# Performance work log

Hardware: AMD Instinct MI355X
Metric: run time of the kernel (lower is better)

The kernel has to match this reference:

```python
import jax, jax.numpy as jnp
import numpy as np

H, W, D = 64, 96, 64          # matching_height, matching_width, num_depth_bins
B, V, C = 1, 4, 16            # batch, num_src_frames, matching feature channels
EPS = 1e-8                    # Project3D eps


def setup_inputs() -> dict:
    key = jax.random.key(0)
    k0, k1, k2 = jax.random.split(key, 3)
    cur_feats = jax.random.normal(k0, (B, C, H, W), jnp.float32)
    src_feats = jax.random.normal(k1, (B, V, C, H, W), jnp.float32)
    # realistic pinhole intrinsics (4x4 homogeneous)
    K = np.eye(4, dtype=np.float32)
    K[0, 0], K[1, 1], K[0, 2], K[1, 2] = 0.9 * W, 1.2 * H, W / 2.0, H / 2.0
    src_Ks = jnp.broadcast_to(jnp.asarray(K), (B, V, 4, 4))
    cur_invK = jnp.broadcast_to(jnp.asarray(np.linalg.inv(K)), (B, 4, 4))
    # near-identity extrinsics (cur cam -> src cam) with small random translations
    t = jax.random.normal(k2, (B, V, 3), jnp.float32) * 0.1
    E = jnp.broadcast_to(jnp.eye(4, dtype=jnp.float32), (B, V, 4, 4))
    src_extrinsics = E.at[:, :, :3, 3].set(t)
    min_depth = jnp.full((B, 1, 1, 1), 0.25, jnp.float32)
    max_depth = jnp.full((B, 1, 1, 1), 5.0, jnp.float32)
    return dict(cur_feats=cur_feats, src_feats=src_feats,
                src_extrinsics=src_extrinsics, src_Ks=src_Ks,
                cur_invK=cur_invK, min_depth=min_depth, max_depth=max_depth)


def _grid_sample_zeros(feat_chw, x, y):
    """torch.grid_sample(mode='bilinear', padding_mode='zeros', align_corners=False)
    for one image. feat_chw: (C,H,W); x,y: (M,) un-normalized pixel coords."""
    f = feat_chw.reshape(feat_chw.shape[0], H * W)  # (C, HW)
    x0, y0 = jnp.floor(x), jnp.floor(y)
    out = jnp.zeros((f.shape[0], x.shape[0]), f.dtype)
    for dx in (0.0, 1.0):
        for dy in (0.0, 1.0):
            xi, yi = x0 + dx, y0 + dy
            w = (1.0 - jnp.abs(x - xi)) * (1.0 - jnp.abs(y - yi))
            valid = (xi >= 0) & (xi < W) & (yi >= 0) & (yi < H)
            idx = (jnp.clip(yi, 0, H - 1) * W + jnp.clip(xi, 0, W - 1)).astype(jnp.int32)
            out = out + f[:, idx] * (w * jnp.where(valid, 1.0, 0.0))[None]
    return out  # (C, M)


def reference(cur_feats, src_feats, src_extrinsics, src_Ks, cur_invK, min_depth, max_depth):
    N = H * W
    # --- generate_depth_planes (log_plane=False -> linear in inverse depth) ---
    ramp = jnp.linspace(0.0, 1.0, D).reshape(1, D)              # linear_ramp
    inv_min = 1.0 / min_depth.reshape(B, 1)
    inv_max = 1.0 / max_depth.reshape(B, 1)
    depth_planes_bd = 1.0 / (inv_min + (inv_max - inv_min) * ramp)  # (B, D)

    # --- BackprojectDepth: pixel grid (+0.5), rays = invK[:3,:3] @ pix ---
    xx, yy = jnp.meshgrid(jnp.arange(W, dtype=jnp.float32) + 0.5,
                          jnp.arange(H, dtype=jnp.float32) + 0.5)
    pix_3N = jnp.stack([xx.ravel(), yy.ravel(), jnp.ones(N, jnp.float32)], 0)
    rays_b3N = jnp.einsum('bij,jn->bin', cur_invK[:, :3, :3], pix_3N)
    world_bd3N = rays_b3N[:, None] * depth_planes_bd[:, :, None, None]   # (B,D,3,N)
    world_bd4N = jnp.concatenate(
        [world_bd3N, jnp.ones((B, D, 1, N), world_bd3N.dtype)], axis=2)

    # --- Project3D: P = K @ T; pix = cam[:2]/(cam[2]+eps) ---
    P_bv34 = jnp.einsum('bvij,bvjk->bvik', src_Ks, src_extrinsics)[:, :, :3]
    cam = jnp.einsum('bvij,bdjn->bvdin', P_bv34, world_bd4N)             # (B,V,D,3,N)
    z = cam[:, :, :, 2]                                                  # (B,V,D,N)
    u = cam[:, :, :, 0] / (z + EPS)
    v = cam[:, :, :, 1] / (z + EPS)

    # uv normalization then grid_sample unnormalization (align_corners=False)
    un = 2.0 * u * (1.0 / W) - 1.0
    vn = 2.0 * v * (1.0 / H) - 1.0
    x = (un + 1.0) * W / 2.0 - 0.5
    y = (vn + 1.0) * H / 2.0 - 0.5

    warped = jax.vmap(_grid_sample_zeros)(
        src_feats.reshape(B * V, C, H, W),
        x.reshape(B * V, D * N), y.reshape(B * V, D * N))                # (BV,C,DN)
    warped = warped.reshape(B, V, C, D, H, W)

    mask = (z > 0).astype(warped.dtype).reshape(B, V, D, H, W)
    # dot over channels with current features, mask, sum over source views
    dot_bvdhw = jnp.einsum('bvcdhw,bchw->bvdhw', warped, cur_feats) * mask
    cost_volume = dot_bvdhw.sum(axis=1)                                  # (B,D,H,W)
    return cost_volume
```

## Files before the change

### kernel.cpp

```cpp
#include <hip/hip_runtime.h>
#include <hip/hip_fp16.h>

#define HH 64
#define WW 96
#define DD 64
#define VV 4
#define CC 16
#define HW (HH*WW)
#define EPSF 1e-8f

typedef _Float16 half2_t __attribute__((ext_vector_type(2)));

#if defined(__has_builtin)
#if __has_builtin(__builtin_amdgcn_fdot2)
#define HAVE_FDOT2 1
#endif
#endif

__device__ __forceinline__ float fdot2_acc(half2_t a, half2_t b, float c) {
#ifdef HAVE_FDOT2
    return __builtin_amdgcn_fdot2(a, b, c, false);
#else
    return c + (float)a.x * (float)b.x + (float)a.y * (float)b.y;
#endif
}

__global__ __launch_bounds__(256) void cv_pack_kernel(
    const float* __restrict__ src, const float* __restrict__ cur,
    __half* __restrict__ srcT, __half* __restrict__ curT)
{
    int tid = blockIdx.x * blockDim.x + threadIdx.x;
    if (tid < VV * HW) {
        int v  = tid / HW;
        int hw = tid - v * HW;
        unsigned short pk[CC];
        #pragma unroll
        for (int c = 0; c < CC; ++c) {
            float f = src[(size_t)v * CC * HW + c * HW + hw];
            pk[c] = __half_as_ushort(__float2half(f));
        }
        uint4* dst = (uint4*)(srcT + (size_t)tid * CC);
        dst[0] = *(uint4*)&pk[0];
        dst[1] = *(uint4*)&pk[8];
    } else {
        int hw = tid - VV * HW;
        if (hw < HW) {
            unsigned short pk[CC];
            #pragma unroll
            for (int c = 0; c < CC; ++c) {
                float f = cur[c * HW + hw];
                pk[c] = __half_as_ushort(__float2half(f));
            }
            uint4* dst = (uint4*)(curT + (size_t)hw * CC);
            dst[0] = *(uint4*)&pk[0];
            dst[1] = *(uint4*)&pk[8];
        }
    }
}

__device__ __forceinline__ float tap_dot16(const __half* __restrict__ p,
                                           const half2_t* __restrict__ cf2)
{
    half2_t hv[8];
    const uint4* q = (const uint4*)p;
    *(uint4*)&hv[0] = q[0];
    *(uint4*)&hv[4] = q[1];
    float s = 0.f;
    #pragma unroll
    for (int i = 0; i < 8; ++i)
        s = fdot2_acc(hv[i], cf2[i], s);
    return s;
}

__global__ __launch_bounds__(256) void cost_volume_f16_kernel(
    const __half* __restrict__ curT,
    const __half* __restrict__ srcT,
    const float* __restrict__ extr,
    const float* __restrict__ Ks,
    const float* __restrict__ invK,
    const float* __restrict__ min_d,
    const float* __restrict__ max_d,
    float* __restrict__ out)
{
    __shared__ float P_s[VV * 12];
    {
        int t = threadIdx.x;
        if (t < VV * 12) {
            int v   = t / 12;
            int r   = (t % 12) / 4;
            int col = t % 4;
            float s = 0.f;
            #pragma unroll
            for (int k = 0; k < 4; ++k)
                s += Ks[v * 16 + r * 4 + k] * extr[v * 16 + k * 4 + col];
            P_s[t] = s;
        }
    }
    __syncthreads();

    int tid = blockIdx.x * blockDim.x + threadIdx.x;
    if (tid >= DD * HW) return;
    int d  = tid / HW;
    int hw = tid - d * HW;
    int h  = hw / WW;
    int w  = hw - h * WW;

    float px = (float)w + 0.5f, py = (float)h + 0.5f;
    float rx = invK[0] * px + invK[1] * py + invK[2];
    float ry = invK[4] * px + invK[5] * py + invK[6];
    float rz = invK[8] * px + invK[9] * py + invK[10];

    float inv_min = 1.f / min_d[0];
    float inv_max = 1.f / max_d[0];
    float depth   = 1.f / (inv_min + (inv_max - inv_min) * ((float)d / (float)(DD - 1)));

    half2_t cf2[8];
    {
        const uint4* p = (const uint4*)(curT + (size_t)hw * CC);
        *(uint4*)&cf2[0] = p[0];
        *(uint4*)&cf2[4] = p[1];
    }

    float acc = 0.f;
    #pragma unroll
    for (int v = 0; v < VV; ++v) {
        const float* P = &P_s[v * 12];
        float cx = depth * (P[0] * rx + P[1] * ry + P[2]  * rz) + P[3];
        float cy = depth * (P[4] * rx + P[5] * ry + P[6]  * rz) + P[7];
        float cz = depth * (P[8] * rx + P[9] * ry + P[10] * rz) + P[11];
        if (cz > 0.f) {
            float iz = 1.f / (cz + EPSF);
            float x = cx * iz - 0.5f;
            float y = cy * iz - 0.5f;
            float x0f = floorf(x), y0f = floorf(y);
            float fx = x - x0f, fy = y - y0f;
            float x1f = x0f + 1.f, y1f = y0f + 1.f;
            int ix0 = (int)fminf(fmaxf(x0f, 0.f), (float)(WW - 1));
            int ix1 = (int)fminf(fmaxf(x1f, 0.f), (float)(WW - 1));
            int iy0 = (int)fminf(fmaxf(y0f, 0.f), (float)(HH - 1));
            int iy1 = (int)fminf(fmaxf(y1f, 0.f), (float)(HH - 1));
            bool vx0 = (x0f >= 0.f) && (x0f < (float)WW);
            bool vx1 = (x1f >= 0.f) && (x1f < (float)WW);
            bool vy0 = (y0f >= 0.f) && (y0f < (float)HH);
            bool vy1 = (y1f >= 0.f) && (y1f < (float)HH);
            float w00 = (vx0 && vy0) ? (1.f - fx) * (1.f - fy) : 0.f;
            float w01 = (vx1 && vy0) ? fx * (1.f - fy) : 0.f;
            float w10 = (vx0 && vy1) ? (1.f - fx) * fy : 0.f;
            float w11 = (vx1 && vy1) ? fx * fy : 0.f;

            const __half* base = srcT + (size_t)v * HW * CC;
            float d00 = tap_dot16(base + (size_t)(iy0 * WW + ix0) * CC, cf2);
            float d01 = tap_dot16(base + (size_t)(iy0 * WW + ix1) * CC, cf2);
            float d10 = tap_dot16(base + (size_t)(iy1 * WW + ix0) * CC, cf2);
            float d11 = tap_dot16(base + (size_t)(iy1 * WW + ix1) * CC, cf2);

            acc += w00 * d00 + w01 * d01 + w10 * d10 + w11 * d11;
        }
    }
    out[tid] = acc;
}

__global__ __launch_bounds__(256) void cost_volume_fallback_kernel(
    const float* __restrict__ curF,
    const float* __restrict__ srcF,
    const float* __restrict__ extr,
    const float* __restrict__ Ks,
    const float* __restrict__ invK,
    const float* __restrict__ min_d,
    const float* __restrict__ max_d,
    float* __restrict__ out)
{
    __shared__ float P_s[VV * 12];
    {
        int t = threadIdx.x;
        if (t < VV * 12) {
            int v   = t / 12;
            int r   = (t % 12) / 4;
            int col = t % 4;
            float s = 0.f;
            #pragma unroll
            for (int k = 0; k < 4; ++k)
                s += Ks[v * 16 + r * 4 + k] * extr[v * 16 + k * 4 + col];
            P_s[t] = s;
        }
    }
    __syncthreads();

    int tid = blockIdx.x * blockDim.x + threadIdx.x;
    if (tid >= DD * HW) return;
    int d  = tid / HW;
    int hw = tid - d * HW;
    int h  = hw / WW;
    int w  = hw - h * WW;

    float px = (float)w + 0.5f, py = (float)h + 0.5f;
    float rx = invK[0] * px + invK[1] * py + invK[2];
    float ry = invK[4] * px + invK[5] * py + invK[6];
    float rz = invK[8] * px + invK[9] * py + invK[10];

    float inv_min = 1.f / min_d[0];
    float inv_max = 1.f / max_d[0];
    float depth   = 1.f / (inv_min + (inv_max - inv_min) * ((float)d / (float)(DD - 1)));

    float cf[CC];
    #pragma unroll
    for (int c = 0; c < CC; ++c) cf[c] = curF[c * HW + hw];

    float acc = 0.f;
    #pragma unroll
    for (int v = 0; v < VV; ++v) {
        const float* P = &P_s[v * 12];
        float cx = depth * (P[0] * rx + P[1] * ry + P[2]  * rz) + P[3];
        float cy = depth * (P[4] * rx + P[5] * ry + P[6]  * rz) + P[7];
        float cz = depth * (P[8] * rx + P[9] * ry + P[10] * rz) + P[11];
        if (cz > 0.f) {
            float iz = 1.f / (cz + EPSF);
            float x = cx * iz - 0.5f;
            float y = cy * iz - 0.5f;
            float x0f = floorf(x), y0f = floorf(y);
            float fx = x - x0f, fy = y - y0f;
            float x1f = x0f + 1.f, y1f = y0f + 1.f;
            int ix0 = (int)fminf(fmaxf(x0f, 0.f), (float)(WW - 1));
            int ix1 = (int)fminf(fmaxf(x1f, 0.f), (float)(WW - 1));
            int iy0 = (int)fminf(fmaxf(y0f, 0.f), (float)(HH - 1));
            int iy1 = (int)fminf(fmaxf(y1f, 0.f), (float)(HH - 1));
            bool vx0 = (x0f >= 0.f) && (x0f < (float)WW);
            bool vx1 = (x1f >= 0.f) && (x1f < (float)WW);
            bool vy0 = (y0f >= 0.f) && (y0f < (float)HH);
            bool vy1 = (y1f >= 0.f) && (y1f < (float)HH);
            float w00 = (vx0 && vy0) ? (1.f - fx) * (1.f - fy) : 0.f;
            float w01 = (vx1 && vy0) ? fx * (1.f - fy) : 0.f;
            float w10 = (vx0 && vy1) ? (1.f - fx) * fy : 0.f;
            float w11 = (vx1 && vy1) ? fx * fy : 0.f;

            float d00 = 0.f, d01 = 0.f, d10 = 0.f, d11 = 0.f;
            int b = v * CC * HW;
            int i00 = iy0 * WW + ix0, i01 = iy0 * WW + ix1;
            int i10 = iy1 * WW + ix0, i11 = iy1 * WW + ix1;
            #pragma unroll
            for (int c = 0; c < CC; ++c) {
                const float* fc = srcF + b + c * HW;
                d00 += fc[i00] * cf[c];
                d01 += fc[i01] * cf[c];
                d10 += fc[i10] * cf[c];
                d11 += fc[i11] * cf[c];
            }
            acc += w00 * d00 + w01 * d01 + w10 * d10 + w11 * d11;
        }
    }
    out[tid] = acc;
}

extern "C" void kernel_launch(void* const* d_in, const int* in_sizes, int n_in,
                              void* d_out, int out_size, void* d_ws, size_t ws_size,
                              hipStream_t stream) {
    const float* cur  = (const float*)d_in[0];
    const float* src  = (const float*)d_in[1];
    const float* extr = (const float*)d_in[2];
    const float* Ks   = (const float*)d_in[3];
    const float* invK = (const float*)d_in[4];
    const float* mind = (const float*)d_in[5];
    const float* maxd = (const float*)d_in[6];
    float* out = (float*)d_out;

    const size_t need = (size_t)(VV * HW * CC + HW * CC) * sizeof(__half);
    const int n_out  = DD * HW;
    const int blocks = (n_out + 255) / 256;

    if (ws_size >= need) {
        __half* srcT = (__half*)d_ws;
        __half* curT = srcT + (size_t)VV * HW * CC;
        const int total = VV * HW + HW;
        cv_pack_kernel<<<(total + 255) / 256, 256, 0, stream>>>(src, cur, srcT, curT);
        cost_volume_f16_kernel<<<blocks, 256, 0, stream>>>(
            curT, srcT, extr, Ks, invK, mind, maxd, out);
    } else {
        cost_volume_fallback_kernel<<<blocks, 256, 0, stream>>>(
            cur, src, extr, Ks, invK, mind, maxd, out);
    }
}
```

Baseline: 76.03 us.

## Process four depth planes per thread to reuse per-pixel setup and current features

Each thread now handles one pixel across four consecutive depth bins, so the ray, the per-view projection terms and the current-feature load are computed once and reused. The block size drops to 128 threads and the grid is re-indexed by depth group and pixel tile. Reciprocals switch to the fast hardware rcp intrinsic, and the cz>0 test becomes a select rather than a branch, so every tap is gathered even for points behind the camera. The trade-offs are higher register pressure, fewer threads in flight, and slightly less precise reciprocals.

```diff
diff --git a/kernel.cpp b/kernel.cpp
--- a/kernel.cpp
+++ b/kernel.cpp
@@ -8,6 +8,9 @@
 #define CC 16
 #define HW (HH*WW)
 #define EPSF 1e-8f
+
+#define DPT 4
+#define MBLK 128
 
 typedef _Float16 half2_t __attribute__((ext_vector_type(2)));
 
@@ -72,7 +75,7 @@
     return s;
 }
 
-__global__ __launch_bounds__(256) void cost_volume_f16_kernel(
+__global__ __launch_bounds__(MBLK) void cost_volume_f16_kernel(
     const __half* __restrict__ curT,
     const __half* __restrict__ srcT,
     const float* __restrict__ extr,
@@ -98,6 +101,111 @@
     }
     __syncthreads();
 
+    const int dg = blockIdx.x / (HW / MBLK);
+    const int hw = (blockIdx.x % (HW / MBLK)) * MBLK + threadIdx.x;
+    const int h  = hw / WW;
+    const int w  = hw - h * WW;
+
+    float px = (float)w + 0.5f, py = (float)h + 0.5f;
+    float rx = invK[0] * px + invK[1] * py + invK[2];
+    float ry = invK[4] * px + invK[5] * py + invK[6];
+    float rz = invK[8] * px + invK[9] * py + invK[10];
+
+    float inv_min = __builtin_amdgcn_rcpf(min_d[0]);
+    float inv_max = __builtin_amdgcn_rcpf(max_d[0]);
+    float dmm = inv_max - inv_min;
+
+    float dep[DPT];
+    #pragma unroll
+    for (int i = 0; i < DPT; ++i) {
+        float fd = (float)(dg * DPT + i) * (1.f / (float)(DD - 1));
+        dep[i] = __builtin_amdgcn_rcpf(inv_min + dmm * fd);
+    }
+
+    half2_t cf2[8];
+    {
+        const uint4* p = (const uint4*)(curT + (size_t)hw * CC);
+        *(uint4*)&cf2[0] = p[0];
+        *(uint4*)&cf2[4] = p[1];
+    }
+
+    float acc[DPT];
+    #pragma unroll
+    for (int i = 0; i < DPT; ++i) acc[i] = 0.f;
+
+    #pragma unroll
+    for (int v = 0; v < VV; ++v) {
+        const float* P = &P_s[v * 12];
+        float a = P[0] * rx + P[1] * ry + P[2]  * rz;
+        float b = P[4] * rx + P[5] * ry + P[6]  * rz;
+        float c = P[8] * rx + P[9] * ry + P[10] * rz;
+        const __half* base = srcT + (size_t)v * HW * CC;
+
+        #pragma unroll
+        for (int i = 0; i < DPT; ++i) {
+            float cz = dep[i] * c + P[11];
+            float cx = dep[i] * a + P[3];
+            float cy = dep[i] * b + P[7];
+            float iz = __builtin_amdgcn_rcpf(cz + EPSF);
+            float x = cx * iz - 0.5f;
+            float y = cy * iz - 0.5f;
+            float x0f = floorf(x), y0f = floorf(y);
+            float fx = x - x0f, fy = y - y0f;
+            float x1f = x0f + 1.f, y1f = y0f + 1.f;
+            int ix0 = (int)fminf(fmaxf(x0f, 0.f), (float)(WW - 1));
+            int ix1 = (int)fminf(fmaxf(x1f, 0.f), (float)(WW - 1));
+            int iy0 = (int)fminf(fmaxf(y0f, 0.f), (float)(HH - 1));
+            int iy1 = (int)fminf(fmaxf(y1f, 0.f), (float)(HH - 1));
+            bool vx0 = (x0f >= 0.f) && (x0f < (float)WW);
+            bool vx1 = (x1f >= 0.f) && (x1f < (float)WW);
+            bool vy0 = (y0f >= 0.f) && (y0f < (float)HH);
+            bool vy1 = (y1f >= 0.f) && (y1f < (float)HH);
+            float w00 = (vx0 && vy0) ? (1.f - fx) * (1.f - fy) : 0.f;
+            float w01 = (vx1 && vy0) ? fx * (1.f - fy) : 0.f;
+            float w10 = (vx0 && vy1) ? (1.f - fx) * fy : 0.f;
+            float w11 = (vx1 && vy1) ? fx * fy : 0.f;
+
+            float d00 = tap_dot16(base + (size_t)(iy0 * WW + ix0) * CC, cf2);
+            float d01 = tap_dot16(base + (size_t)(iy0 * WW + ix1) * CC, cf2);
+            float d10 = tap_dot16(base + (size_t)(iy1 * WW + ix0) * CC, cf2);
+            float d11 = tap_dot16(base + (size_t)(iy1 * WW + ix1) * CC, cf2);
+
+            float vacc = w00 * d00 + w01 * d01 + w10 * d10 + w11 * d11;
+            acc[i] += (cz > 0.f) ? vacc : 0.f;
+        }
+    }
+
+    #pragma unroll
+    for (int i = 0; i < DPT; ++i)
+        out[(size_t)(dg * DPT + i) * HW + hw] = acc[i];
+}
+
+__global__ __launch_bounds__(256) void cost_volume_fallback_kernel(
+    const float* __restrict__ curF,
+    const float* __restrict__ srcF,
+    const float* __restrict__ extr,
+    const float* __restrict__ Ks,
+    const float* __restrict__ invK,
+    const float* __restrict__ min_d,
+    const float* __restrict__ max_d,
+    float* __restrict__ out)
+{
+    __shared__ float P_s[VV * 12];
+    {
+        int t = threadIdx.x;
+        if (t < VV * 12) {
+            int v   = t / 12;
+            int r   = (t % 12) / 4;
+            int col = t % 4;
+            float s = 0.f;
+            #pragma unroll
+            for (int k = 0; k < 4; ++k)
+                s += Ks[v * 16 + r * 4 + k] * extr[v * 16 + k * 4 + col];
+            P_s[t] = s;
+        }
+    }
+    __syncthreads();
+
     int tid = blockIdx.x * blockDim.x + threadIdx.x;
     if (tid >= DD * HW) return;
     int d  = tid / HW;
@@ -114,12 +222,9 @@
     float inv_max = 1.f / max_d[0];
     float depth   = 1.f / (inv_min + (inv_max - inv_min) * ((float)d / (float)(DD - 1)));
 
-    half2_t cf2[8];
-    {
-        const uint4* p = (const uint4*)(curT + (size_t)hw * CC);
-        *(uint4*)&cf2[0] = p[0];
-        *(uint4*)&cf2[4] = p[1];
-    }
+    float cf[CC];
+    #pragma unroll
+    for (int c = 0; c < CC; ++c) cf[c] = curF[c * HW + hw];
 
     float acc = 0.f;
     #pragma unroll
@@ -148,91 +253,6 @@
             float w10 = (vx0 && vy1) ? (1.f - fx) * fy : 0.f;
             float w11 = (vx1 && vy1) ? fx * fy : 0.f;
 
-            const __half* base = srcT + (size_t)v * HW * CC;
-            float d00 = tap_dot16(base + (size_t)(iy0 * WW + ix0) * CC, cf2);
-            float d01 = tap_dot16(base + (size_t)(iy0 * WW + ix1) * CC, cf2);
-            float d10 = tap_dot16(base + (size_t)(iy1 * WW + ix0) * CC, cf2);
-            float d11 = tap_dot16(base + (size_t)(iy1 * WW + ix1) * CC, cf2);
-
-            acc += w00 * d00 + w01 * d01 + w10 * d10 + w11 * d11;
-        }
-    }
-    out[tid] = acc;
-}
-
-__global__ __launch_bounds__(256) void cost_volume_fallback_kernel(
-    const float* __restrict__ curF,
-    const float* __restrict__ srcF,
-    const float* __restrict__ extr,
-    const float* __restrict__ Ks,
-    const float* __restrict__ invK,
-    const float* __restrict__ min_d,
-    const float* __restrict__ max_d,
-    float* __restrict__ out)
-{
-    __shared__ float P_s[VV * 12];
-    {
-        int t = threadIdx.x;
-        if (t < VV * 12) {
-            int v   = t / 12;
-            int r   = (t % 12) / 4;
-            int col = t % 4;
-            float s = 0.f;
-            #pragma unroll
-            for (int k = 0; k < 4; ++k)
-                s += Ks[v * 16 + r * 4 + k] * extr[v * 16 + k * 4 + col];
-            P_s[t] = s;
-        }
-    }
-    __syncthreads();
-
-    int tid = blockIdx.x * blockDim.x + threadIdx.x;
-    if (tid >= DD * HW) return;
-    int d  = tid / HW;
-    int hw = tid - d * HW;
-    int h  = hw / WW;
-    int w  = hw - h * WW;
-
-    float px = (float)w + 0.5f, py = (float)h + 0.5f;
-    float rx = invK[0] * px + invK[1] * py + invK[2];
-    float ry = invK[4] * px + invK[5] * py + invK[6];
-    float rz = invK[8] * px + invK[9] * py + invK[10];
-
-    float inv_min = 1.f / min_d[0];
-    float inv_max = 1.f / max_d[0];
-    float depth   = 1.f / (inv_min + (inv_max - inv_min) * ((float)d / (float)(DD - 1)));
-
-    float cf[CC];
-    #pragma unroll
-    for (int c = 0; c < CC; ++c) cf[c] = curF[c * HW + hw];
-
-    float acc = 0.f;
-    #pragma unroll
-    for (int v = 0; v < VV; ++v) {
-        const float* P = &P_s[v * 12];
-        float cx = depth * (P[0] * rx + P[1] * ry + P[2]  * rz) + P[3];
-        float cy = depth * (P[4] * rx + P[5] * ry + P[6]  * rz) + P[7];
-        float cz = depth * (P[8] * rx + P[9] * ry + P[10] * rz) + P[11];
-        if (cz > 0.f) {
-            float iz = 1.f / (cz + EPSF);
-            float x = cx * iz - 0.5f;
-            float y = cy * iz - 0.5f;
-            float x0f = floorf(x), y0f = floorf(y);
-            float fx = x - x0f, fy = y - y0f;
-            float x1f = x0f + 1.f, y1f = y0f + 1.f;
-            int ix0 = (int)fminf(fmaxf(x0f, 0.f), (float)(WW - 1));
-            int ix1 = (int)fminf(fmaxf(x1f, 0.f), (float)(WW - 1));
-            int iy0 = (int)fminf(fmaxf(y0f, 0.f), (float)(HH - 1));
-            int iy1 = (int)fminf(fmaxf(y1f, 0.f), (float)(HH - 1));
-            bool vx0 = (x0f >= 0.f) && (x0f < (float)WW);
-            bool vx1 = (x1f >= 0.f) && (x1f < (float)WW);
-            bool vy0 = (y0f >= 0.f) && (y0f < (float)HH);
-            bool vy1 = (y1f >= 0.f) && (y1f < (float)HH);
-            float w00 = (vx0 && vy0) ? (1.f - fx) * (1.f - fy) : 0.f;
-            float w01 = (vx1 && vy0) ? fx * (1.f - fy) : 0.f;
-            float w10 = (vx0 && vy1) ? (1.f - fx) * fy : 0.f;
-            float w11 = (vx1 && vy1) ? fx * fy : 0.f;
-
             float d00 = 0.f, d01 = 0.f, d10 = 0.f, d11 = 0.f;
             int b = v * CC * HW;
             int i00 = iy0 * WW + ix0, i01 = iy0 * WW + ix1;
@@ -265,16 +285,17 @@
 
     const size_t need = (size_t)(VV * HW * CC + HW * CC) * sizeof(__half);
     const int n_out  = DD * HW;
-    const int blocks = (n_out + 255) / 256;
 
     if (ws_size >= need) {
         __half* srcT = (__half*)d_ws;
         __half* curT = srcT + (size_t)VV * HW * CC;
         const int total = VV * HW + HW;
         cv_pack_kernel<<<(total + 255) / 256, 256, 0, stream>>>(src, cur, srcT, curT);
-        cost_volume_f16_kernel<<<blocks, 256, 0, stream>>>(
+        const int mblocks = (DD / DPT) * (HW / MBLK);
+        cost_volume_f16_kernel<<<mblocks, MBLK, 0, stream>>>(
             curT, srcT, extr, Ks, invK, mind, maxd, out);
     } else {
+        const int blocks = (n_out + 255) / 256;
         cost_volume_fallback_kernel<<<blocks, 256, 0, stream>>>(
             cur, src, extr, Ks, invK, mind, maxd, out);
     }
```

Result: slower. 81.82 us (+7.6%).

## Map wavefront lanes to depth bins per pixel in f16 cost volume kernel

Applied to the files above, without the earlier changes.

Reassigns threads so each 64-lane wavefront handles one pixel and its lanes cover the 64 depth bins, instead of consecutive pixels at one depth. All lanes then share the current-feature load and ray computation, and the gathered source taps of neighbouring depths cluster along the epipolar line. The cost is output writes strided by HW, which are no longer coalesced. It also swaps divisions for hardware reciprocal approximations and replaces the cz>0 branch with a predicated select to avoid divergence, so all four taps are always fetched.

```diff
diff --git a/kernel.cpp b/kernel.cpp
--- a/kernel.cpp
+++ b/kernel.cpp
@@ -8,6 +8,8 @@
 #define CC 16
 #define HW (HH*WW)
 #define EPSF 1e-8f
+
+#define PIX_PER_BLOCK 4
 
 typedef _Float16 half2_t __attribute__((ext_vector_type(2)));
 
@@ -98,6 +100,100 @@
     }
     __syncthreads();
 
+    const int wv   = threadIdx.x >> 6;
+    const int lane = threadIdx.x & 63;
+    const int hw   = blockIdx.x * PIX_PER_BLOCK + wv;
+    const int h    = hw / WW;
+    const int w    = hw - h * WW;
+    const int d    = lane;
+
+    float px = (float)w + 0.5f, py = (float)h + 0.5f;
+    float rx = invK[0] * px + invK[1] * py + invK[2];
+    float ry = invK[4] * px + invK[5] * py + invK[6];
+    float rz = invK[8] * px + invK[9] * py + invK[10];
+
+    float inv_min = __builtin_amdgcn_rcpf(min_d[0]);
+    float inv_max = __builtin_amdgcn_rcpf(max_d[0]);
+    float depth = __builtin_amdgcn_rcpf(
+        inv_min + (inv_max - inv_min) * ((float)d * (1.f / (float)(DD - 1))));
+
+    half2_t cf2[8];
+    {
+        const uint4* p = (const uint4*)(curT + (size_t)hw * CC);
+        *(uint4*)&cf2[0] = p[0];
+        *(uint4*)&cf2[4] = p[1];
+    }
+
+    float acc = 0.f;
+    #pragma unroll
+    for (int v = 0; v < VV; ++v) {
+        const float* P = &P_s[v * 12];
+        float a = P[0] * rx + P[1] * ry + P[2]  * rz;
+        float b = P[4] * rx + P[5] * ry + P[6]  * rz;
+        float c = P[8] * rx + P[9] * ry + P[10] * rz;
+
+        float cx = depth * a + P[3];
+        float cy = depth * b + P[7];
+        float cz = depth * c + P[11];
+
+        float iz = __builtin_amdgcn_rcpf(cz + EPSF);
+        float x = cx * iz - 0.5f;
+        float y = cy * iz - 0.5f;
+        float x0f = floorf(x), y0f = floorf(y);
+        float fx = x - x0f, fy = y - y0f;
+        float x1f = x0f + 1.f, y1f = y0f + 1.f;
+        int ix0 = (int)fminf(fmaxf(x0f, 0.f), (float)(WW - 1));
+        int ix1 = (int)fminf(fmaxf(x1f, 0.f), (float)(WW - 1));
+        int iy0 = (int)fminf(fmaxf(y0f, 0.f), (float)(HH - 1));
+        int iy1 = (int)fminf(fmaxf(y1f, 0.f), (float)(HH - 1));
+        bool vx0 = (x0f >= 0.f) && (x0f < (float)WW);
+        bool vx1 = (x1f >= 0.f) && (x1f < (float)WW);
+        bool vy0 = (y0f >= 0.f) && (y0f < (float)HH);
+        bool vy1 = (y1f >= 0.f) && (y1f < (float)HH);
+        float w00 = (vx0 && vy0) ? (1.f - fx) * (1.f - fy) : 0.f;
+        float w01 = (vx1 && vy0) ? fx * (1.f - fy) : 0.f;
+        float w10 = (vx0 && vy1) ? (1.f - fx) * fy : 0.f;
+        float w11 = (vx1 && vy1) ? fx * fy : 0.f;
+
+        const __half* base = srcT + (size_t)v * HW * CC;
+        float d00 = tap_dot16(base + (size_t)(iy0 * WW + ix0) * CC, cf2);
+        float d01 = tap_dot16(base + (size_t)(iy0 * WW + ix1) * CC, cf2);
+        float d10 = tap_dot16(base + (size_t)(iy1 * WW + ix0) * CC, cf2);
+        float d11 = tap_dot16(base + (size_t)(iy1 * WW + ix1) * CC, cf2);
+
+        float vacc = w00 * d00 + w01 * d01 + w10 * d10 + w11 * d11;
+        acc += (cz > 0.f) ? vacc : 0.f;
+    }
+
+    out[(size_t)d * HW + hw] = acc;
+}
+
+__global__ __launch_bounds__(256) void cost_volume_fallback_kernel(
+    const float* __restrict__ curF,
+    const float* __restrict__ srcF,
+    const float* __restrict__ extr,
+    const float* __restrict__ Ks,
+    const float* __restrict__ invK,
+    const float* __restrict__ min_d,
+    const float* __restrict__ max_d,
+    float* __restrict__ out)
+{
+    __shared__ float P_s[VV * 12];
+    {
+        int t = threadIdx.x;
+        if (t < VV * 12) {
+            int v   = t / 12;
+            int r   = (t % 12) / 4;
+            int col = t % 4;
+            float s = 0.f;
+            #pragma unroll
+            for (int k = 0; k < 4; ++k)
+                s += Ks[v * 16 + r * 4 + k] * extr[v * 16 + k * 4 + col];
+            P_s[t] = s;
+        }
+    }
+    __syncthreads();
+
     int tid = blockIdx.x * blockDim.x + threadIdx.x;
     if (tid >= DD * HW) return;
     int d  = tid / HW;
@@ -114,12 +210,9 @@
     float inv_max = 1.f / max_d[0];
     float depth   = 1.f / (inv_min + (inv_max - inv_min) * ((float)d / (float)(DD - 1)));
 
-    half2_t cf2[8];
-    {
-        const uint4* p = (const uint4*)(curT + (size_t)hw * CC);
-        *(uint4*)&cf2[0] = p[0];
-        *(uint4*)&cf2[4] = p[1];
-    }
+    float cf[CC];
+    #pragma unroll
+    for (int c = 0; c < CC; ++c) cf[c] = curF[c * HW + hw];
 
     float acc = 0.f;
     #pragma unroll
@@ -148,91 +241,6 @@
             float w10 = (vx0 && vy1) ? (1.f - fx) * fy : 0.f;
             float w11 = (vx1 && vy1) ? fx * fy : 0.f;
 
-            const __half* base = srcT + (size_t)v * HW * CC;
-            float d00 = tap_dot16(base + (size_t)(iy0 * WW + ix0) * CC, cf2);
-            float d01 = tap_dot16(base + (size_t)(iy0 * WW + ix1) * CC, cf2);
-            float d10 = tap_dot16(base + (size_t)(iy1 * WW + ix0) * CC, cf2);
-            float d11 = tap_dot16(base + (size_t)(iy1 * WW + ix1) * CC, cf2);
-
-            acc += w00 * d00 + w01 * d01 + w10 * d10 + w11 * d11;
-        }
-    }
-    out[tid] = acc;
-}
-
-__global__ __launch_bounds__(256) void cost_volume_fallback_kernel(
-    const float* __restrict__ curF,
-    const float* __restrict__ srcF,
-    const float* __restrict__ extr,
-    const float* __restrict__ Ks,
-    const float* __restrict__ invK,
-    const float* __restrict__ min_d,
-    const float* __restrict__ max_d,
-    float* __restrict__ out)
-{
-    __shared__ float P_s[VV * 12];
-    {
-        int t = threadIdx.x;
-        if (t < VV * 12) {
-            int v   = t / 12;
-            int r   = (t % 12) / 4;
-            int col = t % 4;
-            float s = 0.f;
-            #pragma unroll
-            for (int k = 0; k < 4; ++k)
-                s += Ks[v * 16 + r * 4 + k] * extr[v * 16 + k * 4 + col];
-            P_s[t] = s;
-        }
-    }
-    __syncthreads();
-
-    int tid = blockIdx.x * blockDim.x + threadIdx.x;
-    if (tid >= DD * HW) return;
-    int d  = tid / HW;
-    int hw = tid - d * HW;
-    int h  = hw / WW;
-    int w  = hw - h * WW;
-
-    float px = (float)w + 0.5f, py = (float)h + 0.5f;
-    float rx = invK[0] * px + invK[1] * py + invK[2];
-    float ry = invK[4] * px + invK[5] * py + invK[6];
-    float rz = invK[8] * px + invK[9] * py + invK[10];
-
-    float inv_min = 1.f / min_d[0];
-    float inv_max = 1.f / max_d[0];
-    float depth   = 1.f / (inv_min + (inv_max - inv_min) * ((float)d / (float)(DD - 1)));
-
-    float cf[CC];
-    #pragma unroll
-    for (int c = 0; c < CC; ++c) cf[c] = curF[c * HW + hw];
-
-    float acc = 0.f;
-    #pragma unroll
-    for (int v = 0; v < VV; ++v) {
-        const float* P = &P_s[v * 12];
-        float cx = depth * (P[0] * rx + P[1] * ry + P[2]  * rz) + P[3];
-        float cy = depth * (P[4] * rx + P[5] * ry + P[6]  * rz) + P[7];
-        float cz = depth * (P[8] * rx + P[9] * ry + P[10] * rz) + P[11];
-        if (cz > 0.f) {
-            float iz = 1.f / (cz + EPSF);
-            float x = cx * iz - 0.5f;
-            float y = cy * iz - 0.5f;
-            float x0f = floorf(x), y0f = floorf(y);
-            float fx = x - x0f, fy = y - y0f;
-            float x1f = x0f + 1.f, y1f = y0f + 1.f;
-            int ix0 = (int)fminf(fmaxf(x0f, 0.f), (float)(WW - 1));
-            int ix1 = (int)fminf(fmaxf(x1f, 0.f), (float)(WW - 1));
-            int iy0 = (int)fminf(fmaxf(y0f, 0.f), (float)(HH - 1));
-            int iy1 = (int)fminf(fmaxf(y1f, 0.f), (float)(HH - 1));
-            bool vx0 = (x0f >= 0.f) && (x0f < (float)WW);
-            bool vx1 = (x1f >= 0.f) && (x1f < (float)WW);
-            bool vy0 = (y0f >= 0.f) && (y0f < (float)HH);
-            bool vy1 = (y1f >= 0.f) && (y1f < (float)HH);
-            float w00 = (vx0 && vy0) ? (1.f - fx) * (1.f - fy) : 0.f;
-            float w01 = (vx1 && vy0) ? fx * (1.f - fy) : 0.f;
-            float w10 = (vx0 && vy1) ? (1.f - fx) * fy : 0.f;
-            float w11 = (vx1 && vy1) ? fx * fy : 0.f;
-
             float d00 = 0.f, d01 = 0.f, d10 = 0.f, d11 = 0.f;
             int b = v * CC * HW;
             int i00 = iy0 * WW + ix0, i01 = iy0 * WW + ix1;
@@ -265,16 +273,17 @@
 
     const size_t need = (size_t)(VV * HW * CC + HW * CC) * sizeof(__half);
     const int n_out  = DD * HW;
-    const int blocks = (n_out + 255) / 256;
 
     if (ws_size >= need) {
         __half* srcT = (__half*)d_ws;
         __half* curT = srcT + (size_t)VV * HW * CC;
         const int total = VV * HW + HW;
         cv_pack_kernel<<<(total + 255) / 256, 256, 0, stream>>>(src, cur, srcT, curT);
-        cost_volume_f16_kernel<<<blocks, 256, 0, stream>>>(
+        const int mblocks = HW / PIX_PER_BLOCK;
+        cost_volume_f16_kernel<<<mblocks, 256, 0, stream>>>(
             curT, srcT, extr, Ks, invK, mind, maxd, out);
     } else {
+        const int blocks = (n_out + 255) / 256;
         cost_volume_fallback_kernel<<<blocks, 256, 0, stream>>>(
             cur, src, extr, Ks, invK, mind, maxd, out);
     }
```

After: 79.12 us. 1.04x slower.

## Split channel dot across two lanes per output and use fast reciprocals

Applied to the files above, without the earlier changes.

The fp16 cost-volume kernel now assigns two threads to each output, each handling 8 of the 16 channels, and combines them with a lane shuffle. The goal is more parallelism and smaller per-thread gathers (one 16-byte load per tap instead of two), which should help hide the latency of the random bilinear taps. Exact divisions are also replaced with hardware approximate reciprocals. In exchange, the projection and weight math is duplicated across both lanes, there are twice as many threads, and the reciprocals are slightly less precise.

```diff
diff --git a/kernel.cpp b/kernel.cpp
--- a/kernel.cpp
+++ b/kernel.cpp
@@ -58,16 +58,14 @@
     }
 }
 
-__device__ __forceinline__ float tap_dot16(const __half* __restrict__ p,
-                                           const half2_t* __restrict__ cf2)
-{
-    half2_t hv[8];
-    const uint4* q = (const uint4*)p;
-    *(uint4*)&hv[0] = q[0];
-    *(uint4*)&hv[4] = q[1];
+__device__ __forceinline__ float tap_dot8(const __half* __restrict__ p,
+                                          const half2_t* __restrict__ cf2)
+{
+    half2_t hv[4];
+    *(uint4*)&hv[0] = *(const uint4*)p;
     float s = 0.f;
     #pragma unroll
-    for (int i = 0; i < 8; ++i)
+    for (int i = 0; i < 4; ++i)
         s = fdot2_acc(hv[i], cf2[i], s);
     return s;
 }
@@ -98,6 +96,98 @@
     }
     __syncthreads();
 
+    const int tid2    = blockIdx.x * blockDim.x + threadIdx.x;
+    const int out_idx = tid2 >> 1;
+    const int half    = tid2 & 1;
+    const int d  = out_idx / HW;
+    const int hw = out_idx - d * HW;
+    const int h  = hw / WW;
+    const int w  = hw - h * WW;
+
+    float px = (float)w + 0.5f, py = (float)h + 0.5f;
+    float rx = invK[0] * px + invK[1] * py + invK[2];
+    float ry = invK[4] * px + invK[5] * py + invK[6];
+    float rz = invK[8] * px + invK[9] * py + invK[10];
+
+    float inv_min = __builtin_amdgcn_rcpf(min_d[0]);
+    float inv_max = __builtin_amdgcn_rcpf(max_d[0]);
+    float depth = __builtin_amdgcn_rcpf(
+        inv_min + (inv_max - inv_min) * ((float)d * (1.f / (float)(DD - 1))));
+
+    half2_t cf2[4];
+    {
+        const uint4* p = (const uint4*)(curT + (size_t)hw * CC + half * 8);
+        *(uint4*)&cf2[0] = *p;
+    }
+
+    float acc = 0.f;
+    #pragma unroll
+    for (int v = 0; v < VV; ++v) {
+        const float* P = &P_s[v * 12];
+        float cx = depth * (P[0] * rx + P[1] * ry + P[2]  * rz) + P[3];
+        float cy = depth * (P[4] * rx + P[5] * ry + P[6]  * rz) + P[7];
+        float cz = depth * (P[8] * rx + P[9] * ry + P[10] * rz) + P[11];
+        if (cz > 0.f) {
+            float iz = __builtin_amdgcn_rcpf(cz + EPSF);
+            float x = cx * iz - 0.5f;
+            float y = cy * iz - 0.5f;
+            float x0f = floorf(x), y0f = floorf(y);
+            float fx = x - x0f, fy = y - y0f;
+            float x1f = x0f + 1.f, y1f = y0f + 1.f;
+            int ix0 = (int)fminf(fmaxf(x0f, 0.f), (float)(WW - 1));
+            int ix1 = (int)fminf(fmaxf(x1f, 0.f), (float)(WW - 1));
+            int iy0 = (int)fminf(fmaxf(y0f, 0.f), (float)(HH - 1));
+            int iy1 = (int)fminf(fmaxf(y1f, 0.f), (float)(HH - 1));
+            bool vx0 = (x0f >= 0.f) && (x0f < (float)WW);
+            bool vx1 = (x1f >= 0.f) && (x1f < (float)WW);
+            bool vy0 = (y0f >= 0.f) && (y0f < (float)HH);
+            bool vy1 = (y1f >= 0.f) && (y1f < (float)HH);
+            float w00 = (vx0 && vy0) ? (1.f - fx) * (1.f - fy) : 0.f;
+            float w01 = (vx1 && vy0) ? fx * (1.f - fy) : 0.f;
+            float w10 = (vx0 && vy1) ? (1.f - fx) * fy : 0.f;
+            float w11 = (vx1 && vy1) ? fx * fy : 0.f;
+
+            const __half* base = srcT + (size_t)v * HW * CC + half * 8;
+            float d00 = tap_dot8(base + (size_t)(iy0 * WW + ix0) * CC, cf2);
+            float d01 = tap_dot8(base + (size_t)(iy0 * WW + ix1) * CC, cf2);
+            float d10 = tap_dot8(base + (size_t)(iy1 * WW + ix0) * CC, cf2);
+            float d11 = tap_dot8(base + (size_t)(iy1 * WW + ix1) * CC, cf2);
+
+            acc += w00 * d00 + w01 * d01 + w10 * d10 + w11 * d11;
+        }
+    }
+
+    acc += __shfl_xor(acc, 1, 64);
+    if (half == 0)
+        out[out_idx] = acc;
+}
+
+__global__ __launch_bounds__(256) void cost_volume_fallback_kernel(
+    const float* __restrict__ curF,
+    const float* __restrict__ srcF,
+    const float* __restrict__ extr,
+    const float* __restrict__ Ks,
+    const float* __restrict__ invK,
+    const float* __restrict__ min_d,
+    const float* __restrict__ max_d,
+    float* __restrict__ out)
+{
+    __shared__ float P_s[VV * 12];
+    {
+        int t = threadIdx.x;
+        if (t < VV * 12) {
+            int v   = t / 12;
+            int r   = (t % 12) / 4;
+            int col = t % 4;
+            float s = 0.f;
+            #pragma unroll
+            for (int k = 0; k < 4; ++k)
+                s += Ks[v * 16 + r * 4 + k] * extr[v * 16 + k * 4 + col];
+            P_s[t] = s;
+        }
+    }
+    __syncthreads();
+
     int tid = blockIdx.x * blockDim.x + threadIdx.x;
     if (tid >= DD * HW) return;
     int d  = tid / HW;
@@ -114,12 +204,9 @@
     float inv_max = 1.f / max_d[0];
     float depth   = 1.f / (inv_min + (inv_max - inv_min) * ((float)d / (float)(DD - 1)));
 
-    half2_t cf2[8];
-    {
-        const uint4* p = (const uint4*)(curT + (size_t)hw * CC);
-        *(uint4*)&cf2[0] = p[0];
-        *(uint4*)&cf2[4] = p[1];
-    }
+    float cf[CC];
+    #pragma unroll
+    for (int c = 0; c < CC; ++c) cf[c] = curF[c * HW + hw];
 
     float acc = 0.f;
     #pragma unroll
@@ -148,91 +235,6 @@
             float w10 = (vx0 && vy1) ? (1.f - fx) * fy : 0.f;
             float w11 = (vx1 && vy1) ? fx * fy : 0.f;
 
-            const __half* base = srcT + (size_t)v * HW * CC;
-            float d00 = tap_dot16(base + (size_t)(iy0 * WW + ix0) * CC, cf2);
-            float d01 = tap_dot16(base + (size_t)(iy0 * WW + ix1) * CC, cf2);
-            float d10 = tap_dot16(base + (size_t)(iy1 * WW + ix0) * CC, cf2);
-            float d11 = tap_dot16(base + (size_t)(iy1 * WW + ix1) * CC, cf2);
-
-            acc += w00 * d00 + w01 * d01 + w10 * d10 + w11 * d11;
-        }
-    }
-    out[tid] = acc;
-}
-
-__global__ __launch_bounds__(256) void cost_volume_fallback_kernel(
-    const float* __restrict__ curF,
-    const float* __restrict__ srcF,
-    const float* __restrict__ extr,
-    const float* __restrict__ Ks,
-    const float* __restrict__ invK,
-    const float* __restrict__ min_d,
-    const float* __restrict__ max_d,
-    float* __restrict__ out)
-{
-    __shared__ float P_s[VV * 12];
-    {
-        int t = threadIdx.x;
-        if (t < VV * 12) {
-            int v   = t / 12;
-            int r   = (t % 12) / 4;
-            int col = t % 4;
-            float s = 0.f;
-            #pragma unroll
-            for (int k = 0; k < 4; ++k)
-                s += Ks[v * 16 + r * 4 + k] * extr[v * 16 + k * 4 + col];
-            P_s[t] = s;
-        }
-    }
-    __syncthreads();
-
-    int tid = blockIdx.x * blockDim.x + threadIdx.x;
-    if (tid >= DD * HW) return;
-    int d  = tid / HW;
-    int hw = tid - d * HW;
-    int h  = hw / WW;
-    int w  = hw - h * WW;
-
-    float px = (float)w + 0.5f, py = (float)h + 0.5f;
-    float rx = invK[0] * px + invK[1] * py + invK[2];
-    float ry = invK[4] * px + invK[5] * py + invK[6];
-    float rz = invK[8] * px + invK[9] * py + invK[10];
-
-    float inv_min = 1.f / min_d[0];
-    float inv_max = 1.f / max_d[0];
-    float depth   = 1.f / (inv_min + (inv_max - inv_min) * ((float)d / (float)(DD - 1)));
-
-    float cf[CC];
-    #pragma unroll
-    for (int c = 0; c < CC; ++c) cf[c] = curF[c * HW + hw];
-
-    float acc = 0.f;
-    #pragma unroll
-    for (int v = 0; v < VV; ++v) {
-        const float* P = &P_s[v * 12];
-        float cx = depth * (P[0] * rx + P[1] * ry + P[2]  * rz) + P[3];
-        float cy = depth * (P[4] * rx + P[5] * ry + P[6]  * rz) + P[7];
-        float cz = depth * (P[8] * rx + P[9] * ry + P[10] * rz) + P[11];
-        if (cz > 0.f) {
-            float iz = 1.f / (cz + EPSF);
-            float x = cx * iz - 0.5f;
-            float y = cy * iz - 0.5f;
-            float x0f = floorf(x), y0f = floorf(y);
-            float fx = x - x0f, fy = y - y0f;
-            float x1f = x0f + 1.f, y1f = y0f + 1.f;
-            int ix0 = (int)fminf(fmaxf(x0f, 0.f), (float)(WW - 1));
-            int ix1 = (int)fminf(fmaxf(x1f, 0.f), (float)(WW - 1));
-            int iy0 = (int)fminf(fmaxf(y0f, 0.f), (float)(HH - 1));
-            int iy1 = (int)fminf(fmaxf(y1f, 0.f), (float)(HH - 1));
-            bool vx0 = (x0f >= 0.f) && (x0f < (float)WW);
-            bool vx1 = (x1f >= 0.f) && (x1f < (float)WW);
-            bool vy0 = (y0f >= 0.f) && (y0f < (float)HH);
-            bool vy1 = (y1f >= 0.f) && (y1f < (float)HH);
-            float w00 = (vx0 && vy0) ? (1.f - fx) * (1.f - fy) : 0.f;
-            float w01 = (vx1 && vy0) ? fx * (1.f - fy) : 0.f;
-            float w10 = (vx0 && vy1) ? (1.f - fx) * fy : 0.f;
-            float w11 = (vx1 && vy1) ? fx * fy : 0.f;
-
             float d00 = 0.f, d01 = 0.f, d10 = 0.f, d11 = 0.f;
             int b = v * CC * HW;
             int i00 = iy0 * WW + ix0, i01 = iy0 * WW + ix1;
@@ -265,16 +267,17 @@
 
     const size_t need = (size_t)(VV * HW * CC + HW * CC) * sizeof(__half);
     const int n_out  = DD * HW;
-    const int blocks = (n_out + 255) / 256;
 
     if (ws_size >= need) {
         __half* srcT = (__half*)d_ws;
         __half* curT = srcT + (size_t)VV * HW * CC;
         const int total = VV * HW + HW;
         cv_pack_kernel<<<(total + 255) / 256, 256, 0, stream>>>(src, cur, srcT, curT);
-        cost_volume_f16_kernel<<<blocks, 256, 0, stream>>>(
+        const int mblocks = (DD * HW * 2) / 256;
+        cost_volume_f16_kernel<<<mblocks, 256, 0, stream>>>(
             curT, srcT, extr, Ks, invK, mind, maxd, out);
     } else {
+        const int blocks = (n_out + 255) / 256;
         cost_volume_fallback_kernel<<<blocks, 256, 0, stream>>>(
             cur, src, extr, Ks, invK, mind, maxd, out);
     }
```

New measurement: 79.01 us. +3.9%, slower.
